# Performance work log

Measured on AMD Instinct MI355X. Metric: run time of the kernel, lower is better.

## Reference

```python
import jax, jax.numpy as jnp
import numpy as np

N_U, N_I, D, Q, NNZ, L = 100000, 100000, 64, 128, 3200000, 3
N = N_U + N_I

def setup_inputs() -> dict:
    key = jax.random.key(0)
    ks = jax.random.split(key, 9)
    user_emb = jax.random.normal(ks[0], (N_U, D), dtype=jnp.float32) * 0.1
    item_emb = jax.random.normal(ks[1], (N_I, D), dtype=jnp.float32) * 0.1
    adj_row = jax.random.randint(ks[2], (NNZ,), 0, N, dtype=jnp.int32)
    adj_col = jax.random.randint(ks[3], (NNZ,), 0, N, dtype=jnp.int32)
    # ~degree-normalized values so L-layer propagation stays stable
    adj_vals = jax.random.uniform(ks[4], (NNZ,), dtype=jnp.float32) / 16.0
    ut = jax.random.normal(ks[5], (Q, N_U), dtype=jnp.float32) * (1.0 / np.sqrt(N_U))
    vt = jax.random.normal(ks[6], (Q, N_I), dtype=jnp.float32) * (1.0 / np.sqrt(N_I))
    u_mul_s = jax.random.normal(ks[7], (N_U, Q), dtype=jnp.float32) * 0.1
    v_mul_s = jax.random.normal(ks[8], (N_I, Q), dtype=jnp.float32) * 0.1
    return {"user_emb": user_emb, "item_emb": item_emb, "adj_row": adj_row,
            "adj_col": adj_col, "adj_vals": adj_vals, "ut": ut, "vt": vt,
            "u_mul_s": u_mul_s, "v_mul_s": v_mul_s}

def _spmm(row, col, vals, x):
    # y[r] = sum_{e: row[e]==r} vals[e] * x[col[e]]
    return jax.ops.segment_sum(vals[:, None] * x[col], row, num_segments=N)

def reference(user_emb, item_emb, adj_row, adj_col, adj_vals, ut, vt, u_mul_s, v_mul_s):
    ego = jnp.concatenate([user_emb, item_emb], axis=0)  # [N, D]
    acc = jnp.zeros_like(ego)
    svd_u = jnp.zeros((N_U, D), dtype=ego.dtype)
    svd_i = jnp.zeros((N_I, D), dtype=ego.dtype)
    for _ in range(L):
        ego = _spmm(adj_row, adj_col, adj_vals, ego)
        acc = acc + ego
        ue, ie = ego[:N_U], ego[N_U:]
        ut_eu = ut @ ue            # [Q, D]
        vt_ei = vt @ ie            # [Q, D]
        svd_u = svd_u + u_mul_s @ vt_ei
        svd_i = svd_i + v_mul_s @ ut_eu
    mean = acc / L                 # mean over stacked layer embeddings
    return (mean[:N_U], svd_u, mean[N_U:], svd_i)
```

## Files before the change

### kernel.cpp

```cpp
#include <hip/hip_runtime.h>

constexpr int N_U  = 100000;
constexpr int N_I  = 100000;
constexpr int NTOT = 200000;
constexpr int D    = 64;
constexpr int Q    = 128;
constexpr int NNZ  = 3200000;
constexpr int SEG  = N_U * D;

constexpr int G1_CHUNK = 400;
constexpr int G1_NBLK  = 250;

constexpr int BROWS   = 512;
constexpr int NBUCK   = (NTOT + BROWS - 1) / BROWS;
constexpr int P_CHUNK = 8192;
constexpr int P_NBLK  = (NNZ + P_CHUNK - 1) / P_CHUNK;

constexpr int G2_ROWS = 64;
constexpr int G2_NBLK = (N_U + G2_ROWS - 1) / G2_ROWS;

constexpr int CVT_CNT  = NTOT * D / 8;
constexpr int CVT_BLKS = (CVT_CNT + 511) / 512;

__device__ __forceinline__ unsigned short f2bf(float f) {
  unsigned int b = __float_as_uint(f);
  return (unsigned short)((b + 0x7fff + ((b >> 16) & 1)) >> 16);
}
__device__ __forceinline__ float bf2f(unsigned short u) {
  return __uint_as_float((unsigned int)u << 16);
}

__global__ void __launch_bounds__(512) k_pre(const int* __restrict__ row,
                                             int* __restrict__ part,
                                             const float* __restrict__ user_emb,
                                             const float* __restrict__ item_emb,
                                             unsigned short* __restrict__ e0) {
  __shared__ int h[NBUCK];
  const int t = threadIdx.x;
  if (blockIdx.x < (unsigned)P_NBLK) {
    if (t < NBUCK) h[t] = 0;
    __syncthreads();
    const int e0i = blockIdx.x * P_CHUNK;
#pragma unroll
    for (int i = 0; i < P_CHUNK / 512; ++i) {
      int e = e0i + i * 512 + t;
      if (e < NNZ) atomicAdd(&h[row[e] >> 9], 1);
    }
    __syncthreads();
    if (t < NBUCK) part[blockIdx.x * NBUCK + t] = h[t];
  } else {
    int i = (blockIdx.x - P_NBLK) * 512 + t;
    if (i >= CVT_CNT) return;
    size_t base = (size_t)i * 8;
    const float* src = (base < (size_t)SEG) ? (user_emb + base) : (item_emb + base - SEG);
    float4 v0 = *reinterpret_cast<const float4*>(src);
    float4 v1 = *reinterpret_cast<const float4*>(src + 4);
    union { unsigned short us[8]; uint4 u4; } pk;
    pk.us[0] = f2bf(v0.x); pk.us[1] = f2bf(v0.y); pk.us[2] = f2bf(v0.z); pk.us[3] = f2bf(v0.w);
    pk.us[4] = f2bf(v1.x); pk.us[5] = f2bf(v1.y); pk.us[6] = f2bf(v1.z); pk.us[7] = f2bf(v1.w);
    *reinterpret_cast<uint4*>(e0 + base) = pk.u4;
  }
}

__global__ void __launch_bounds__(64) k_bscanA(const int* __restrict__ part,
                                               int* __restrict__ outb,
                                               int* __restrict__ btot) {
  const int b = blockIdx.x;
  const int l = threadIdx.x;
  int carry = 0;
#pragma unroll
  for (int round = 0; round < (P_NBLK + 63) / 64; ++round) {
    int blk = round * 64 + l;
    int v = (blk < P_NBLK) ? part[blk * NBUCK + b] : 0;
    int x = v;
#pragma unroll
    for (int off = 1; off < 64; off <<= 1) {
      int y = __shfl_up(x, off, 64);
      if (l >= off) x += y;
    }
    if (blk < P_NBLK) outb[blk * NBUCK + b] = carry + x - v;
    carry += __shfl(x, 63, 64);
  }
  if (l == 0) btot[b] = carry;
}

__global__ void __launch_bounds__(512) k_bscanB(const int* __restrict__ btot,
                                                int* __restrict__ bbase) {
  __shared__ int s[512];
  const int t = threadIdx.x;
  const int own = (t < NBUCK) ? btot[t] : 0;
  s[t] = own;
  __syncthreads();
  for (int off = 1; off < 512; off <<= 1) {
    int y = (t >= off) ? s[t - off] : 0;
    __syncthreads();
    s[t] += y;
    __syncthreads();
  }
  if (t <= NBUCK) bbase[t] = s[t] - own;
}

__global__ void __launch_bounds__(512) k_mscat(const int* __restrict__ row,
                                               const int* __restrict__ col,
                                               const float* __restrict__ val,
                                               const int* __restrict__ outb,
                                               const int* __restrict__ bbase,
                                               int2* __restrict__ ebuck) {
  __shared__ int cur[NBUCK];
  const int t = threadIdx.x;
  if (t < NBUCK) cur[t] = bbase[t] + outb[blockIdx.x * NBUCK + t];
  __syncthreads();
  const int e0 = blockIdx.x * P_CHUNK;
#pragma unroll
  for (int i = 0; i < P_CHUNK / 512; ++i) {
    int e = e0 + i * 512 + t;
    if (e < NNZ) {
      int r = row[e];
      int b = r >> 9;
      int pos = atomicAdd(&cur[b], 1);
      ebuck[pos] = make_int2(col[e] | ((r & (BROWS - 1)) << 18), __float_as_int(val[e]));
    }
  }
}

__global__ void __launch_bounds__(512) k_rsort(const int* __restrict__ bbase,
                                               const int2* __restrict__ ebuck,
                                               int2* __restrict__ edges,
                                               int* __restrict__ rowptr) {
  __shared__ int s[512];
  __shared__ int cur[512];
  const int t = threadIdx.x;
  const int b = blockIdx.x;
  const int eb0 = bbase[b], eb1 = bbase[b + 1];
  cur[t] = 0;
  __syncthreads();
  for (int e = eb0 + t; e < eb1; e += 512) atomicAdd(&cur[ebuck[e].x >> 18], 1);
  __syncthreads();
  const int own = cur[t];
  s[t] = own;
  __syncthreads();
  for (int off = 1; off < 512; off <<= 1) {
    int y = (t >= off) ? s[t - off] : 0;
    __syncthreads();
    s[t] += y;
    __syncthreads();
  }
  const int excl = s[t] - own;
  const int r = (b << 9) + t;
  if (r < NTOT) rowptr[r] = eb0 + excl;
  if (b == NBUCK - 1 && t == 0) rowptr[NTOT] = NNZ;
  cur[t] = eb0 + excl;
  __syncthreads();
  for (int e = eb0 + t; e < eb1; e += 512) {
    int2 kv = ebuck[e];
    int pos = atomicAdd(&cur[kv.x >> 18], 1);
    edges[pos] = make_int2(kv.x & 0x3FFFF, kv.y);
  }
}

template <int FINAL>
__global__ void k_spmm(const int* __restrict__ rowptr, const int2* __restrict__ edges,
                       const unsigned short* __restrict__ src,
                       unsigned short* __restrict__ dst,
                       const unsigned short* __restrict__ p1,
                       const unsigned short* __restrict__ p2,
                       float* __restrict__ mean_u, float* __restrict__ mean_i) {
  const int r = (blockIdx.x * 256 + threadIdx.x) >> 6;
  const int lane = threadIdx.x & 63;
  if (r >= NTOT) return;
  const int eb = rowptr[r], ee = rowptr[r + 1];
  float sA = 0.f, sB = 0.f;
  int e = eb;
#define GIDX(dd) ((unsigned)(((dd).x << 6) + lane))
  for (; e + 16 <= ee; e += 16) {
    int2 d0 = edges[e + 0], d1 = edges[e + 1], d2 = edges[e + 2], d3 = edges[e + 3];
    int2 d4 = edges[e + 4], d5 = edges[e + 5], d6 = edges[e + 6], d7 = edges[e + 7];
    int2 d8 = edges[e + 8], d9 = edges[e + 9], da = edges[e + 10], db = edges[e + 11];
    int2 dc = edges[e + 12], dd = edges[e + 13], de = edges[e + 14], df = edges[e + 15];
    unsigned short u0 = src[GIDX(d0)], u1 = src[GIDX(d1)], u2 = src[GIDX(d2)], u3 = src[GIDX(d3)];
    unsigned short u4 = src[GIDX(d4)], u5 = src[GIDX(d5)], u6 = src[GIDX(d6)], u7 = src[GIDX(d7)];
    unsigned short u8 = src[GIDX(d8)], u9 = src[GIDX(d9)], ua = src[GIDX(da)], ub = src[GIDX(db)];
    unsigned short uc = src[GIDX(dc)], ud = src[GIDX(dd)], ue = src[GIDX(de)], uf = src[GIDX(df)];
    sA = fmaf(__int_as_float(d0.y), bf2f(u0), sA);
    sB = fmaf(__int_as_float(d1.y), bf2f(u1), sB);
    sA = fmaf(__int_as_float(d2.y), bf2f(u2), sA);
    sB = fmaf(__int_as_float(d3.y), bf2f(u3), sB);
    sA = fmaf(__int_as_float(d4.y), bf2f(u4), sA);
    sB = fmaf(__int_as_float(d5.y), bf2f(u5), sB);
    sA = fmaf(__int_as_float(d6.y), bf2f(u6), sA);
    sB = fmaf(__int_as_float(d7.y), bf2f(u7), sB);
    sA = fmaf(__int_as_float(d8.y), bf2f(u8), sA);
    sB = fmaf(__int_as_float(d9.y), bf2f(u9), sB);
    sA = fmaf(__int_as_float(da.y), bf2f(ua), sA);
    sB = fmaf(__int_as_float(db.y), bf2f(ub), sB);
    sA = fmaf(__int_as_float(dc.y), bf2f(uc), sA);
    sB = fmaf(__int_as_float(dd.y), bf2f(ud), sB);
    sA = fmaf(__int_as_float(de.y), bf2f(ue), sA);
    sB = fmaf(__int_as_float(df.y), bf2f(uf), sB);
  }
  for (; e + 4 <= ee; e += 4) {
    int2 d0 = edges[e + 0], d1 = edges[e + 1], d2 = edges[e + 2], d3 = edges[e + 3];
    unsigned short u0 = src[GIDX(d0)], u1 = src[GIDX(d1)], u2 = src[GIDX(d2)], u3 = src[GIDX(d3)];
    sA = fmaf(__int_as_float(d0.y), bf2f(u0), sA);
    sB = fmaf(__int_as_float(d1.y), bf2f(u1), sB);
    sA = fmaf(__int_as_float(d2.y), bf2f(u2), sA);
    sB = fmaf(__int_as_float(d3.y), bf2f(u3), sB);
  }
  for (; e < ee; ++e) {
    int2 d0 = edges[e];
    sA = fmaf(__int_as_float(d0.y), bf2f(src[GIDX(d0)]), sA);
  }
#undef GIDX
  const float sum = sA + sB;
  const unsigned idx = ((unsigned)r << 6) + lane;
  if (!FINAL) {
    __builtin_nontemporal_store(f2bf(sum), &dst[idx]);
  } else {
    float m = (bf2f(p1[idx]) + bf2f(p2[idx]) + sum) * (1.f / 3.f);
    if (r < N_U) mean_u[idx] = m;
    else         mean_i[idx - (unsigned)SEG] = m;
  }
}

__global__ void __launch_bounds__(512) k_g1(const float* __restrict__ ut,
                                            const float* __restrict__ vt,
                                            const float* __restrict__ accu,
                                            const float* __restrict__ acci,
                                            float* __restrict__ Ppart) {
  __shared__ float Wl[128 * 65];
  __shared__ float Xl[64 * 64];
  const int mat = blockIdx.y;
  const float* __restrict__ W = mat ? vt : ut;
  const float* __restrict__ X = mat ? acci : accu;
  const int t = threadIdx.x;
  const int q0 = (t >> 4) * 4;
  const int d0 = (t & 15) * 4;
  const int n0 = blockIdx.x * G1_CHUNK;
  const int n1 = min(n0 + G1_CHUNK, N_U);
  float4 a0 = {0, 0, 0, 0}, a1 = {0, 0, 0, 0}, a2 = {0, 0, 0, 0}, a3 = {0, 0, 0, 0};
  for (int k = n0; k < n1; k += 64) {
#pragma unroll
    for (int rep = 0; rep < 2; ++rep) {
      int f4 = t + rep * 512;
      int row = f4 >> 4;
      int c4 = (f4 & 15) * 4;
      int gr = k + row;
      float4 v = (gr < n1) ? *reinterpret_cast<const float4*>(X + (size_t)gr * 64 + c4)
                           : float4{0, 0, 0, 0};
      *reinterpret_cast<float4*>(&Xl[row * 64 + c4]) = v;
    }
    {
      int q = t >> 2;
      int c16 = (t & 3) * 16;
#pragma unroll
      for (int jj = 0; jj < 4; ++jj) {
        int kk = c16 + jj * 4;
        int gk = k + kk;
        float4 v = (gk < n1) ? *reinterpret_cast<const float4*>(W + (size_t)q * N_U + gk)
                             : float4{0, 0, 0, 0};
        *reinterpret_cast<float4*>(&Wl[q * 65 + kk]) = v;
      }
    }
    __syncthreads();
#pragma unroll 2
    for (int kk = 0; kk < 64; kk += 4) {
      float4 w0 = *reinterpret_cast<const float4*>(&Wl[(q0 + 0) * 65 + kk]);
      float4 w1 = *reinterpret_cast<const float4*>(&Wl[(q0 + 1) * 65 + kk]);
      float4 w2 = *reinterpret_cast<const float4*>(&Wl[(q0 + 2) * 65 + kk]);
      float4 w3 = *reinterpret_cast<const float4*>(&Wl[(q0 + 3) * 65 + kk]);
      float4 x0 = *reinterpret_cast<const float4*>(&Xl[(kk + 0) * 64 + d0]);
      float4 x1 = *reinterpret_cast<const float4*>(&Xl[(kk + 1) * 64 + d0]);
      float4 x2 = *reinterpret_cast<const float4*>(&Xl[(kk + 2) * 64 + d0]);
      float4 x3 = *reinterpret_cast<const float4*>(&Xl[(kk + 3) * 64 + d0]);
#define FMA16(aj, wj)                                                                 \
  aj.x = fmaf(wj.x, x0.x, aj.x); aj.y = fmaf(wj.x, x0.y, aj.y);                       \
  aj.z = fmaf(wj.x, x0.z, aj.z); aj.w = fmaf(wj.x, x0.w, aj.w);                       \
  aj.x = fmaf(wj.y, x1.x, aj.x); aj.y = fmaf(wj.y, x1.y, aj.y);                       \
  aj.z = fmaf(wj.y, x1.z, aj.z); aj.w = fmaf(wj.y, x1.w, aj.w);                       \
  aj.x = fmaf(wj.z, x2.x, aj.x); aj.y = fmaf(wj.z, x2.y, aj.y);                       \
  aj.z = fmaf(wj.z, x2.z, aj.z); aj.w = fmaf(wj.z, x2.w, aj.w);                       \
  aj.x = fmaf(wj.w, x3.x, aj.x); aj.y = fmaf(wj.w, x3.y, aj.y);                       \
  aj.z = fmaf(wj.w, x3.z, aj.z); aj.w = fmaf(wj.w, x3.w, aj.w);
      FMA16(a0, w0)
      FMA16(a1, w1)
      FMA16(a2, w2)
      FMA16(a3, w3)
#undef FMA16
    }
    __syncthreads();
  }
  float* dst = Ppart + ((size_t)mat * G1_NBLK + blockIdx.x) * (Q * D);
  *reinterpret_cast<float4*>(dst + (q0 + 0) * 64 + d0) = a0;
  *reinterpret_cast<float4*>(dst + (q0 + 1) * 64 + d0) = a1;
  *reinterpret_cast<float4*>(dst + (q0 + 2) * 64 + d0) = a2;
  *reinterpret_cast<float4*>(dst + (q0 + 3) * 64 + d0) = a3;
}

__global__ void k_reduce(const float* __restrict__ Ppart, float* __restrict__ P) {
  int idx = blockIdx.x * 256 + threadIdx.x;
  if (idx >= 2 * Q * D) return;
  int mat = idx >> 13;
  int qd = idx & (Q * D - 1);
  const float* src = Ppart + (size_t)mat * G1_NBLK * (Q * D) + qd;
  float s = 0.f;
#pragma unroll 4
  for (int b = 0; b < G1_NBLK; ++b) s += src[(size_t)b * (Q * D)];
  P[idx] = s * 3.f;
}

__global__ void __launch_bounds__(256) k_g2(const float* __restrict__ u_mul_s,
                                            const float* __restrict__ v_mul_s,
                                            const float* __restrict__ P,
                                            float* __restrict__ svd_u,
                                            float* __restrict__ svd_i) {
  __shared__ float Pl[Q * D];
  const int mat = blockIdx.y;
  const float* __restrict__ M  = mat ? v_mul_s : u_mul_s;
  const float* __restrict__ Pg = mat ? P : (P + Q * D);
  float* __restrict__ outp     = mat ? svd_i : svd_u;
  const int t = threadIdx.x;
#pragma unroll
  for (int i = 0; i < 8; ++i) {
    int idx = i * 256 + t;
    reinterpret_cast<float4*>(Pl)[idx] = reinterpret_cast<const float4*>(Pg)[idx];
  }
  __syncthreads();
  const int c0 = (t & 15) * 4;
  const int rbase = blockIdx.x * G2_ROWS + (t >> 4) * 4;
  const float4* mr0 = reinterpret_cast<const float4*>(M + (size_t)(rbase + 0 < N_U ? rbase + 0 : 0) * Q);
  const float4* mr1 = reinterpret_cast<const float4*>(M + (size_t)(rbase + 1 < N_U ? rbase + 1 : 0) * Q);
  const float4* mr2 = reinterpret_cast<const float4*>(M + (size_t)(rbase + 2 < N_U ? rbase + 2 : 0) * Q);
  const float4* mr3 = reinterpret_cast<const float4*>(M + (size_t)(rbase + 3 < N_U ? rbase + 3 : 0) * Q);
  float4 a0 = {0, 0, 0, 0}, a1 = {0, 0, 0, 0}, a2 = {0, 0, 0, 0}, a3 = {0, 0, 0, 0};
#pragma unroll 4
  for (int k4 = 0; k4 < Q / 4; ++k4) {
    float4 m0 = mr0[k4];
    float4 m1 = mr1[k4];
    float4 m2 = mr2[k4];
    float4 m3 = mr3[k4];
    float4 p0 = *reinterpret_cast<const float4*>(&Pl[(k4 * 4 + 0) * D + c0]);
    float4 p1 = *reinterpret_cast<const float4*>(&Pl[(k4 * 4 + 1) * D + c0]);
    float4 p2 = *reinterpret_cast<const float4*>(&Pl[(k4 * 4 + 2) * D + c0]);
    float4 p3 = *reinterpret_cast<const float4*>(&Pl[(k4 * 4 + 3) * D + c0]);
#define G2FMA(aj, mj)                                                                 \
  aj.x = fmaf(mj.x, p0.x, aj.x); aj.y = fmaf(mj.x, p0.y, aj.y);                       \
  aj.z = fmaf(mj.x, p0.z, aj.z); aj.w = fmaf(mj.x, p0.w, aj.w);                       \
  aj.x = fmaf(mj.y, p1.x, aj.x); aj.y = fmaf(mj.y, p1.y, aj.y);                       \
  aj.z = fmaf(mj.y, p1.z, aj.z); aj.w = fmaf(mj.y, p1.w, aj.w);                       \
  aj.x = fmaf(mj.z, p2.x, aj.x); aj.y = fmaf(mj.z, p2.y, aj.y);                       \
  aj.z = fmaf(mj.z, p2.z, aj.z); aj.w = fmaf(mj.z, p2.w, aj.w);                       \
  aj.x = fmaf(mj.w, p3.x, aj.x); aj.y = fmaf(mj.w, p3.y, aj.y);                       \
  aj.z = fmaf(mj.w, p3.z, aj.z); aj.w = fmaf(mj.w, p3.w, aj.w);
    G2FMA(a0, m0)
    G2FMA(a1, m1)
    G2FMA(a2, m2)
    G2FMA(a3, m3)
#undef G2FMA
  }
  if (rbase + 0 < N_U) *reinterpret_cast<float4*>(outp + (size_t)(rbase + 0) * D + c0) = a0;
  if (rbase + 1 < N_U) *reinterpret_cast<float4*>(outp + (size_t)(rbase + 1) * D + c0) = a1;
  if (rbase + 2 < N_U) *reinterpret_cast<float4*>(outp + (size_t)(rbase + 2) * D + c0) = a2;
  if (rbase + 3 < N_U) *reinterpret_cast<float4*>(outp + (size_t)(rbase + 3) * D + c0) = a3;
}

extern "C" void kernel_launch(void* const* d_in, const int* in_sizes, int n_in,
                              void* d_out, int out_size, void* d_ws, size_t ws_size,
                              hipStream_t stream) {
  const float* user_emb = (const float*)d_in[0];
  const float* item_emb = (const float*)d_in[1];
  const int*   adj_row  = (const int*)d_in[2];
  const int*   adj_col  = (const int*)d_in[3];
  const float* adj_vals = (const float*)d_in[4];
  const float* ut       = (const float*)d_in[5];
  const float* vt       = (const float*)d_in[6];
  const float* u_mul_s  = (const float*)d_in[7];
  const float* v_mul_s  = (const float*)d_in[8];
  float* out = (float*)d_out;

  char* ws = (char*)d_ws;
  size_t off = 0;
  auto alloc = [&](size_t bytes) -> void* {
    void* p = ws + off;
    off = (off + bytes + 255) & ~(size_t)255;
    return p;
  };
  unsigned short* eb0 = (unsigned short*)alloc((size_t)NTOT * D * 2);
  unsigned short* eb1 = (unsigned short*)alloc((size_t)NTOT * D * 2);
  unsigned short* eb2 = (unsigned short*)alloc((size_t)NTOT * D * 2);
  int2*  ebuck  = (int2*)alloc((size_t)NNZ * 8);
  int2*  edges  = (int2*)alloc((size_t)NNZ * 8);
  int*   rowptr = (int*)alloc((size_t)(NTOT + 1) * 4);
  int*   part   = (int*)alloc((size_t)P_NBLK * NBUCK * 4);
  int*   outb   = (int*)alloc((size_t)P_NBLK * NBUCK * 4);
  int*   btot   = (int*)alloc((size_t)NBUCK * 4);
  int*   bbase  = (int*)alloc((size_t)(NBUCK + 1) * 4);
  float* P      = (float*)alloc(2 * Q * D * 4);
  float* Ppart  = (float*)alloc((size_t)2 * G1_NBLK * Q * D * 4);

  float* mean_u = out;
  float* svd_u  = out + (size_t)SEG;
  float* mean_i = out + 2 * (size_t)SEG;
  float* svd_i  = out + 3 * (size_t)SEG;

  k_pre<<<P_NBLK + CVT_BLKS, 512, 0, stream>>>(adj_row, part, user_emb, item_emb, eb0);
  k_bscanA<<<NBUCK, 64, 0, stream>>>(part, outb, btot);
  k_bscanB<<<1, 512, 0, stream>>>(btot, bbase);
  k_mscat<<<P_NBLK, 512, 0, stream>>>(adj_row, adj_col, adj_vals, outb, bbase, ebuck);
  k_rsort<<<NBUCK, 512, 0, stream>>>(bbase, ebuck, edges, rowptr);

  const int spmmGrid = (NTOT * 64) / 256;
  k_spmm<0><<<spmmGrid, 256, 0, stream>>>(rowptr, edges, eb0, eb1, nullptr, nullptr,
                                          nullptr, nullptr);
  k_spmm<0><<<spmmGrid, 256, 0, stream>>>(rowptr, edges, eb1, eb2, nullptr, nullptr,
                                          nullptr, nullptr);
  k_spmm<1><<<spmmGrid, 256, 0, stream>>>(rowptr, edges, eb2, nullptr, eb1, eb2,
                                          mean_u, mean_i);

  k_g1<<<dim3(G1_NBLK, 2), 512, 0, stream>>>(ut, vt, mean_u, mean_i, Ppart);
  k_reduce<<<(2 * Q * D + 255) / 256, 256, 0, stream>>>(Ppart, P);

  k_g2<<<dim3(G2_NBLK, 2), 256, 0, stream>>>(u_mul_s, v_mul_s, P, svd_u, svd_i);
}
```

Before: 635.8 us.

## Process two SpMM rows per wavefront with packed bf16x2 gathers

The SpMM kernel now assigns 32 lanes per row, so each wavefront handles two rows. Each lane gathers one 32-bit word holding two bf16 features instead of a single 16-bit value. This halves the number of gather instructions and edge-list reads per row. Edges are read as 64-bit nontemporal loads and the unroll drops from 16 to 8. The grid is halved to match, and the final layer writes two floats per lane.

Measured after the change: 578.4 us. -9.0%, faster.

```diff
diff --git a/kernel.cpp b/kernel.cpp
--- a/kernel.cpp
+++ b/kernel.cpp
@@ -29,6 +29,8 @@
 __device__ __forceinline__ float bf2f(unsigned short u) {
   return __uint_as_float((unsigned int)u << 16);
 }
+__device__ __forceinline__ float bflo(unsigned u) { return __uint_as_float(u << 16); }
+__device__ __forceinline__ float bfhi(unsigned u) { return __uint_as_float(u & 0xffff0000u); }
 
 __global__ void __launch_bounds__(512) k_pre(const int* __restrict__ row,
                                              int* __restrict__ part,
@@ -159,66 +161,68 @@
 }
 
 template <int FINAL>
-__global__ void k_spmm(const int* __restrict__ rowptr, const int2* __restrict__ edges,
-                       const unsigned short* __restrict__ src,
-                       unsigned short* __restrict__ dst,
-                       const unsigned short* __restrict__ p1,
-                       const unsigned short* __restrict__ p2,
-                       float* __restrict__ mean_u, float* __restrict__ mean_i) {
-  const int r = (blockIdx.x * 256 + threadIdx.x) >> 6;
-  const int lane = threadIdx.x & 63;
+__global__ void __launch_bounds__(256) k_spmm(
+    const int* __restrict__ rowptr, const int2* __restrict__ edges,
+    const unsigned* __restrict__ src32, unsigned* __restrict__ dst32,
+    const unsigned* __restrict__ p1, const unsigned* __restrict__ p2,
+    float* __restrict__ mean_u, float* __restrict__ mean_i) {
+  const int wid = (blockIdx.x * 256 + threadIdx.x) >> 6;
+  const int half = (threadIdx.x >> 5) & 1;
+  const int l = threadIdx.x & 31;
+  const int r = wid * 2 + half;
   if (r >= NTOT) return;
   const int eb = rowptr[r], ee = rowptr[r + 1];
-  float sA = 0.f, sB = 0.f;
+  const unsigned long long* __restrict__ e64 =
+      reinterpret_cast<const unsigned long long*>(edges);
+  float s0 = 0.f, s1 = 0.f;
   int e = eb;
-#define GIDX(dd) ((unsigned)(((dd).x << 6) + lane))
-  for (; e + 16 <= ee; e += 16) {
-    int2 d0 = edges[e + 0], d1 = edges[e + 1], d2 = edges[e + 2], d3 = edges[e + 3];
-    int2 d4 = edges[e + 4], d5 = edges[e + 5], d6 = edges[e + 6], d7 = edges[e + 7];
-    int2 d8 = edges[e + 8], d9 = edges[e + 9], da = edges[e + 10], db = edges[e + 11];
-    int2 dc = edges[e + 12], dd = edges[e + 13], de = edges[e + 14], df = edges[e + 15];
-    unsigned short u0 = src[GIDX(d0)], u1 = src[GIDX(d1)], u2 = src[GIDX(d2)], u3 = src[GIDX(d3)];
-    unsigned short u4 = src[GIDX(d4)], u5 = src[GIDX(d5)], u6 = src[GIDX(d6)], u7 = src[GIDX(d7)];
-    unsigned short u8 = src[GIDX(d8)], u9 = src[GIDX(d9)], ua = src[GIDX(da)], ub = src[GIDX(db)];
-    unsigned short uc = src[GIDX(dc)], ud = src[GIDX(dd)], ue = src[GIDX(de)], uf = src[GIDX(df)];
-    sA = fmaf(__int_as_float(d0.y), bf2f(u0), sA);
-    sB = fmaf(__int_as_float(d1.y), bf2f(u1), sB);
-    sA = fmaf(__int_as_float(d2.y), bf2f(u2), sA);
-    sB = fmaf(__int_as_float(d3.y), bf2f(u3), sB);
-    sA = fmaf(__int_as_float(d4.y), bf2f(u4), sA);
-    sB = fmaf(__int_as_float(d5.y), bf2f(u5), sB);
-    sA = fmaf(__int_as_float(d6.y), bf2f(u6), sA);
-    sB = fmaf(__int_as_float(d7.y), bf2f(u7), sB);
-    sA = fmaf(__int_as_float(d8.y), bf2f(u8), sA);
-    sB = fmaf(__int_as_float(d9.y), bf2f(u9), sB);
-    sA = fmaf(__int_as_float(da.y), bf2f(ua), sA);
-    sB = fmaf(__int_as_float(db.y), bf2f(ub), sB);
-    sA = fmaf(__int_as_float(dc.y), bf2f(uc), sA);
-    sB = fmaf(__int_as_float(dd.y), bf2f(ud), sB);
-    sA = fmaf(__int_as_float(de.y), bf2f(ue), sA);
-    sB = fmaf(__int_as_float(df.y), bf2f(uf), sB);
-  }
-  for (; e + 4 <= ee; e += 4) {
-    int2 d0 = edges[e + 0], d1 = edges[e + 1], d2 = edges[e + 2], d3 = edges[e + 3];
-    unsigned short u0 = src[GIDX(d0)], u1 = src[GIDX(d1)], u2 = src[GIDX(d2)], u3 = src[GIDX(d3)];
-    sA = fmaf(__int_as_float(d0.y), bf2f(u0), sA);
-    sB = fmaf(__int_as_float(d1.y), bf2f(u1), sB);
-    sA = fmaf(__int_as_float(d2.y), bf2f(u2), sA);
-    sB = fmaf(__int_as_float(d3.y), bf2f(u3), sB);
-  }
-  for (; e < ee; ++e) {
-    int2 d0 = edges[e];
-    sA = fmaf(__int_as_float(d0.y), bf2f(src[GIDX(d0)]), sA);
-  }
-#undef GIDX
-  const float sum = sA + sB;
-  const unsigned idx = ((unsigned)r << 6) + lane;
+#define EDGE(q) unsigned long long q
+#define LD(q, i) q = __builtin_nontemporal_load(&e64[e + i])
+#define GA(u, q) unsigned u = src32[(((unsigned)(unsigned int)(q)) << 5) + l]
+#define FMA(q, u)                                                     \
+  {                                                                   \
+    float v = __uint_as_float((unsigned)((q) >> 32));                 \
+    s0 = fmaf(v, bflo(u), s0);                                        \
+    s1 = fmaf(v, bfhi(u), s1);                                        \
+  }
+  for (; e + 8 <= ee; e += 8) {
+    EDGE(q0); EDGE(q1); EDGE(q2); EDGE(q3); EDGE(q4); EDGE(q5); EDGE(q6); EDGE(q7);
+    LD(q0, 0); LD(q1, 1); LD(q2, 2); LD(q3, 3);
+    LD(q4, 4); LD(q5, 5); LD(q6, 6); LD(q7, 7);
+    GA(u0, q0); GA(u1, q1); GA(u2, q2); GA(u3, q3);
+    GA(u4, q4); GA(u5, q5); GA(u6, q6); GA(u7, q7);
+    FMA(q0, u0) FMA(q1, u1) FMA(q2, u2) FMA(q3, u3)
+    FMA(q4, u4) FMA(q5, u5) FMA(q6, u6) FMA(q7, u7)
+  }
+  for (; e + 2 <= ee; e += 2) {
+    EDGE(q0); EDGE(q1);
+    LD(q0, 0); LD(q1, 1);
+    GA(u0, q0); GA(u1, q1);
+    FMA(q0, u0) FMA(q1, u1)
+  }
+  if (e < ee) {
+    EDGE(q0);
+    LD(q0, 0);
+    GA(u0, q0);
+    FMA(q0, u0)
+  }
+#undef EDGE
+#undef LD
+#undef GA
+#undef FMA
+  const unsigned idx = ((unsigned)r << 5) + l;
   if (!FINAL) {
-    __builtin_nontemporal_store(f2bf(sum), &dst[idx]);
+    unsigned pk = (unsigned)f2bf(s0) | ((unsigned)f2bf(s1) << 16);
+    __builtin_nontemporal_store(pk, &dst32[idx]);
   } else {
-    float m = (bf2f(p1[idx]) + bf2f(p2[idx]) + sum) * (1.f / 3.f);
-    if (r < N_U) mean_u[idx] = m;
-    else         mean_i[idx - (unsigned)SEG] = m;
+    unsigned a = __builtin_nontemporal_load(&p1[idx]);
+    unsigned b = __builtin_nontemporal_load(&p2[idx]);
+    float m0 = (bflo(a) + bflo(b) + s0) * (1.f / 3.f);
+    float m1 = (bfhi(a) + bfhi(b) + s1) * (1.f / 3.f);
+    float* dstp = (r < N_U) ? (mean_u + ((size_t)r << 6) + l * 2)
+                            : (mean_i + (((size_t)(r - N_U)) << 6) + l * 2);
+    dstp[0] = m0;
+    dstp[1] = m1;
   }
 }
 
@@ -408,13 +412,16 @@
   k_mscat<<<P_NBLK, 512, 0, stream>>>(adj_row, adj_col, adj_vals, outb, bbase, ebuck);
   k_rsort<<<NBUCK, 512, 0, stream>>>(bbase, ebuck, edges, rowptr);
 
-  const int spmmGrid = (NTOT * 64) / 256;
-  k_spmm<0><<<spmmGrid, 256, 0, stream>>>(rowptr, edges, eb0, eb1, nullptr, nullptr,
+  const int spmmGrid = (NTOT * 64) / 512;
+  k_spmm<0><<<spmmGrid, 256, 0, stream>>>(rowptr, edges, (const unsigned*)eb0,
+                                          (unsigned*)eb1, nullptr, nullptr,
                                           nullptr, nullptr);
-  k_spmm<0><<<spmmGrid, 256, 0, stream>>>(rowptr, edges, eb1, eb2, nullptr, nullptr,
+  k_spmm<0><<<spmmGrid, 256, 0, stream>>>(rowptr, edges, (const unsigned*)eb1,
+                                          (unsigned*)eb2, nullptr, nullptr,
                                           nullptr, nullptr);
-  k_spmm<1><<<spmmGrid, 256, 0, stream>>>(rowptr, edges, eb2, nullptr, eb1, eb2,
-                                          mean_u, mean_i);
+  k_spmm<1><<<spmmGrid, 256, 0, stream>>>(rowptr, edges, (const unsigned*)eb2,
+                                          nullptr, (const unsigned*)eb1,
+                                          (const unsigned*)eb2, mean_u, mean_i);
 
   k_g1<<<dim3(G1_NBLK, 2), 512, 0, stream>>>(ut, vt, mean_u, mean_i, Ppart);
   k_reduce<<<(2 * Q * D + 255) / 256, 256, 0, stream>>>(Ppart, P);
```
